# Kernel optimization log

Hardware: AMD Instinct MI355X
Metric: run time of the kernel (lower is better)

## Reference

```python
import jax, jax.numpy as jnp
import numpy as np

N, IN_DIM, H, D = 4096, 512, 8, 64
NEG = -1e9  # additive mask value for non-edges


def setup_inputs() -> dict:
    key = jax.random.key(0)
    k1, k2, k3, k4, k5, k6 = jax.random.split(key, 6)
    data = jax.random.normal(k1, (N, IN_DIM), dtype=jnp.float32)
    r = jax.random.uniform(k2, (N, N), dtype=jnp.float32)
    connectivity = jnp.where(r < 0.05, 0.0, NEG).astype(jnp.float32)
    # xavier-uniform-ish init for params
    lim_w = float(np.sqrt(6.0 / (IN_DIM + H * D)))
    W = jax.random.uniform(k3, (H * D, IN_DIM), jnp.float32, -lim_w, lim_w)
    b = jnp.zeros((H * D,), jnp.float32)
    lim_p = float(np.sqrt(6.0 / (H * D + 1)))
    src_proj = jax.random.uniform(k4, (1, H, D), jnp.float32, -lim_p, lim_p)
    trg_proj = jax.random.uniform(k5, (1, H, D), jnp.float32, -lim_p, lim_p)
    return {"data": data, "connectivity": connectivity, "W": W, "b": b,
            "src_proj": src_proj, "trg_proj": trg_proj}


def reference(data, connectivity, W, b, src_proj, trg_proj):
    # dropout is identity in eval mode (reference is deterministic)
    data1 = (data @ W.T + b).reshape(N, H, D)          # (N,H,D)
    src = jnp.einsum('nhd,xhd->nh', data1, src_proj)   # (N,H)
    trg = jnp.einsum('nhd,xhd->nh', data1, trg_proj)   # (N,H)
    # scores: (H,N,1) + (H,1,N) broadcast outer-sum
    e = src.T[:, :, None] + trg.T[:, None, :]          # (H,N,N)
    e = jnp.where(e >= 0, e, 0.01 * e)                 # LeakyReLU(0.01)
    e = e + connectivity[None, :, :]                   # additive mask
    scores = jax.nn.softmax(e, axis=-1)                # (H,N,N)
    # bmm over heads: (H,N,N) x (H,N,D) -> (H,N,D)
    out = jnp.einsum('hnm,hmd->hnd', scores, data1.transpose(1, 0, 2))
    out = out.transpose(1, 0, 2).reshape(N, H * D)     # concat=True
    return out
```

## Files before the change

kernel.cpp:

```cpp
#include <hip/hip_runtime.h>
#include <hip/hip_bf16.h>

#define NN 4096
#define IN_DIM 512
#define NH 8
#define DD 64
#define HD 512
#define LOG2E 1.4426950408889634f
#define CAST_WGS 2304
#define SCAN_WGS 1024


typedef __attribute__((ext_vector_type(8))) short short8;
typedef __attribute__((ext_vector_type(4))) float f32x4;

static __device__ __forceinline__ unsigned short f2bf(float x) {
    __hip_bfloat16 h = __float2bfloat16(x);
    return *reinterpret_cast<unsigned short*>(&h);
}

static __device__ __forceinline__ unsigned cvtpk_bf16(float a, float b) {
    unsigned r;
    asm("v_cvt_pk_bf16_f32 %0, %1, %2" : "=v"(r) : "v"(a), "v"(b));
    return r;
}

__global__ __launch_bounds__(256) void k_cast_scan(const float* __restrict__ inA,
                                                   unsigned short* __restrict__ outA,
                                                   int n4A,
                                                   const float* __restrict__ inB,
                                                   unsigned short* __restrict__ outB,
                                                   int n4B,
                                                   const float* __restrict__ conn,
                                                   unsigned long long* __restrict__ bm) {
    if (blockIdx.x >= CAST_WGS) {
        const int lane = threadIdx.x & 63;
        const int w = threadIdx.x >> 6;
        const int row = (blockIdx.x - CAST_WGS) * 4 + w;
        const float* crow = conn + (size_t)row * NN;
        unsigned long long keep = 0;
#pragma unroll 8
        for (int t = 0; t < 64; t++) {
            float c = crow[t * 64 + lane];
            unsigned long long m = __ballot(c == 0.0f);
            if (lane == t) keep = m;
        }
        bm[(size_t)row * 64 + lane] = keep;
        return;
    }
    int t = blockIdx.x * 256 + threadIdx.x;
    const float* in;
    unsigned short* out;
    if (t < n4A) {
        in = inA; out = outA;
    } else {
        t -= n4A;
        if (t >= n4B) return;
        in = inB; out = outB;
    }
    float4 v = ((const float4*)in)[t];
    ushort4 o;
    o.x = f2bf(v.x); o.y = f2bf(v.y); o.z = f2bf(v.z); o.w = f2bf(v.w);
    ((ushort4*)out)[t] = o;
}

__global__ __launch_bounds__(512) void k_gemm_fused(const unsigned short* __restrict__ Ab,
                                                    const unsigned short* __restrict__ Wb,
                                                    const float* __restrict__ bias,
                                                    const float* __restrict__ sp,
                                                    const float* __restrict__ tp,
                                                    unsigned short* __restrict__ d1t,
                                                    float* __restrict__ srcT,
                                                    float* __restrict__ trgT) {
    __shared__ f32x4 cbuf[4][4 * 64];
    const int lane = threadIdx.x & 63;
    const int w8 = threadIdx.x >> 6;
    const int w  = w8 & 3;
    const int kh = w8 >> 2;
    const int col = lane & 15;
    const int quad = lane >> 4;
    const int koff = quad * 8 + kh * 256;
    const int h = blockIdx.x;
    const int m0 = h * 64;
    const int n0 = blockIdx.y * 64;

    const short8* ap  = (const short8*)(Ab + (size_t)(n0 + w * 16 + col) * IN_DIM + koff);
    const short8* bp0 = (const short8*)(Wb + (size_t)(m0 +  0 + col) * IN_DIM + koff);
    const short8* bp1 = (const short8*)(Wb + (size_t)(m0 + 16 + col) * IN_DIM + koff);
    const short8* bp2 = (const short8*)(Wb + (size_t)(m0 + 32 + col) * IN_DIM + koff);
    const short8* bp3 = (const short8*)(Wb + (size_t)(m0 + 48 + col) * IN_DIM + koff);

    f32x4 acc0 = {0.f, 0.f, 0.f, 0.f}, acc1 = acc0, acc2 = acc0, acc3 = acc0;

#pragma unroll 8
    for (int ks = 0; ks < 8; ks++) {
        short8 a  = ap[ks * 4];
        short8 b0 = bp0[ks * 4];
        short8 b1 = bp1[ks * 4];
        short8 b2 = bp2[ks * 4];
        short8 b3 = bp3[ks * 4];
        acc0 = __builtin_amdgcn_mfma_f32_16x16x32_bf16(a, b0, acc0, 0, 0, 0);
        acc1 = __builtin_amdgcn_mfma_f32_16x16x32_bf16(a, b1, acc1, 0, 0, 0);
        acc2 = __builtin_amdgcn_mfma_f32_16x16x32_bf16(a, b2, acc2, 0, 0, 0);
        acc3 = __builtin_amdgcn_mfma_f32_16x16x32_bf16(a, b3, acc3, 0, 0, 0);
    }

    if (kh == 1) {
        cbuf[w][0 * 64 + lane] = acc0;
        cbuf[w][1 * 64 + lane] = acc1;
        cbuf[w][2 * 64 + lane] = acc2;
        cbuf[w][3 * 64 + lane] = acc3;
    }
    __syncthreads();
    if (kh == 1) return;
    acc0 += cbuf[w][0 * 64 + lane];
    acc1 += cbuf[w][1 * 64 + lane];
    acc2 += cbuf[w][2 * 64 + lane];
    acc3 += cbuf[w][3 * 64 + lane];

    const int rbase = n0 + w * 16 + quad * 4;
    const int jt  = (n0 >> 5) + (w >> 1);
    const int kqf = ((w & 1) << 1) + (quad >> 1);
    const int half = quad & 1;
    f32x4 accs[4] = {acc0, acc1, acc2, acc3};
    float ps[4] = {0.f, 0.f, 0.f, 0.f};
    float pt[4] = {0.f, 0.f, 0.f, 0.f};
#pragma unroll
    for (int mt = 0; mt < 4; mt++) {
        const int m = m0 + mt * 16 + col;
        const float bv  = bias[m];
        const float spv = sp[m];
        const float tpv = tp[m];
        ushort4 pack;
        unsigned short* pk = (unsigned short*)&pack;
#pragma unroll
        for (int r = 0; r < 4; r++) {
            float v = accs[mt][r] + bv;
            pk[r] = f2bf(v);
            ps[r] += v * spv;
            pt[r] += v * tpv;
        }
        size_t boff = ((((size_t)(h * 128 + jt) * 4 + mt) * 64 + kqf * 16 + col) << 4)
                    + ((size_t)half << 3);
        *(ushort4*)((char*)d1t + boff) = pack;
    }
#pragma unroll
    for (int off = 1; off <= 8; off <<= 1) {
#pragma unroll
        for (int r = 0; r < 4; r++) {
            ps[r] += __shfl_xor(ps[r], off, 64);
            pt[r] += __shfl_xor(pt[r], off, 64);
        }
    }
    if (col < 4)
        srcT[(size_t)h * NN + rbase + col] = ps[col] * LOG2E;
    else if (col < 8)
        trgT[(size_t)h * NN + rbase + col - 4] = pt[col - 4] * LOG2E;
}

__global__ __launch_bounds__(512) void k_flash(const unsigned* __restrict__ bm32,
                                               const float* __restrict__ srcT,
                                               const float* __restrict__ trgT,
                                               const unsigned short* __restrict__ d1t,
                                               float* __restrict__ out) {
    __shared__ char vt[2][16384];

    const int t = threadIdx.x;
    const int lane = t & 63;
    const int w = t >> 6;
    const int col = lane & 15;
    const int kq = lane >> 4;
    const int i0 = blockIdx.x * 128;
    const int h = blockIdx.y;
    const int m = i0 + w * 16 + col;

    const float s = srcT[(size_t)h * NN + m];
    const unsigned* bp = bm32 + (size_t)m * 128;
    const float* tpp = trgT + (size_t)h * NN + kq * 8;
    const uint4* gv = (const uint4*)d1t + (size_t)h * 32768;
    const short8 ONES = {0x3F80, 0x3F80, 0x3F80, 0x3F80, 0x3F80, 0x3F80, 0x3F80, 0x3F80};

    f32x4 acc0 = {0.f, 0.f, 0.f, 0.f}, acc1 = acc0, acc2 = acc0, acc3 = acc0;
    f32x4 asum = acc0;

    {
        uint4 a0 = gv[t];
        uint4 a1 = gv[t + 512];
        *(uint4*)(vt[0] + (size_t)t * 16) = a0;
        *(uint4*)(vt[0] + (size_t)(t + 512) * 16) = a1;
    }
    uint4 st0 = gv[1024 + t];
    uint4 st1 = gv[1024 + t + 512];
    uint4 bq_c = *(const uint4*)(bp);
    uint4 bq_n = *(const uint4*)(bp + 4);
    float4 tAc[4], tBc[4], tAn[4], tBn[4];
#pragma unroll
    for (int jtl = 0; jtl < 4; jtl++) {
        tAc[jtl] = *(const float4*)(tpp + jtl * 32);
        tBc[jtl] = *(const float4*)(tpp + jtl * 32 + 4);
        tAn[jtl] = *(const float4*)(tpp + (4 + jtl) * 32);
        tBn[jtl] = *(const float4*)(tpp + (4 + jtl) * 32 + 4);
    }
    __syncthreads();

#pragma unroll 2
    for (int step = 0; step < 32; step++) {
        const int cur = step & 1;
        char* wb = vt[cur ^ 1];
        *(uint4*)(wb + (size_t)t * 16) = st0;
        *(uint4*)(wb + (size_t)(t + 512) * 16) = st1;
        const int s2 = (step + 2 < 32) ? step + 2 : 31;
        st0 = gv[s2 * 1024 + t];
        st1 = gv[s2 * 1024 + t + 512];

        const unsigned bqa[4] = {bq_c.x, bq_c.y, bq_c.z, bq_c.w};
#pragma unroll
        for (int jtl = 0; jtl < 4; jtl++) {
            const unsigned bits = (bqa[jtl] >> (kq * 8)) & 0xffu;
            const float tv[8] = {tAc[jtl].x, tAc[jtl].y, tAc[jtl].z, tAc[jtl].w,
                                 tBc[jtl].x, tBc[jtl].y, tBc[jtl].z, tBc[jtl].w};
            float p[8];
#pragma unroll
            for (int r = 0; r < 8; r++) {
                float e = s + tv[r];
                e = fmaxf(e, 0.01f * e);
                float pv = __builtin_amdgcn_exp2f(e);
                pv *= (float)((bits >> r) & 1u);
                p[r] = pv;
            }
            union { uint4 u; short8 s8; } pk;
            pk.u.x = cvtpk_bf16(p[0], p[1]);
            pk.u.y = cvtpk_bf16(p[2], p[3]);
            pk.u.z = cvtpk_bf16(p[4], p[5]);
            pk.u.w = cvtpk_bf16(p[6], p[7]);
            const char* cb = vt[cur] + jtl * 4096 + lane * 16;
            short8 v0 = *(const short8*)(cb);
            short8 v1 = *(const short8*)(cb + 1024);
            short8 v2 = *(const short8*)(cb + 2048);
            short8 v3 = *(const short8*)(cb + 3072);
            acc0 = __builtin_amdgcn_mfma_f32_16x16x32_bf16(pk.s8, v0, acc0, 0, 0, 0);
            acc1 = __builtin_amdgcn_mfma_f32_16x16x32_bf16(pk.s8, v1, acc1, 0, 0, 0);
            acc2 = __builtin_amdgcn_mfma_f32_16x16x32_bf16(pk.s8, v2, acc2, 0, 0, 0);
            acc3 = __builtin_amdgcn_mfma_f32_16x16x32_bf16(pk.s8, v3, acc3, 0, 0, 0);
            asum = __builtin_amdgcn_mfma_f32_16x16x32_bf16(pk.s8, ONES, asum, 0, 0, 0);
        }

        bq_c = bq_n;
#pragma unroll
        for (int jtl = 0; jtl < 4; jtl++) { tAc[jtl] = tAn[jtl]; tBc[jtl] = tBn[jtl]; }
        bq_n = *(const uint4*)(bp + s2 * 4);
#pragma unroll
        for (int jtl = 0; jtl < 4; jtl++) {
            tAn[jtl] = *(const float4*)(tpp + (s2 * 4 + jtl) * 32);
            tBn[jtl] = *(const float4*)(tpp + (s2 * 4 + jtl) * 32 + 4);
        }
        __syncthreads();
    }

    f32x4 accs[4] = {acc0, acc1, acc2, acc3};
#pragma unroll
    for (int r = 0; r < 4; r++) {
        const int row = i0 + w * 16 + kq * 4 + r;
        const float dv = asum[r];
        const float inv = (dv > 0.f) ? (1.f / dv) : 0.f;
        float* op = out + (size_t)row * HD + h * 64;
#pragma unroll
        for (int dt = 0; dt < 4; dt++)
            op[dt * 16 + col] = accs[dt][r] * inv;
    }
}

extern "C" void kernel_launch(void* const* d_in, const int* in_sizes, int n_in,
                              void* d_out, int out_size, void* d_ws, size_t ws_size,
                              hipStream_t stream) {
    const float* data = (const float*)d_in[0];
    const float* conn = (const float*)d_in[1];
    const float* W    = (const float*)d_in[2];
    const float* bias = (const float*)d_in[3];
    const float* sp   = (const float*)d_in[4];
    const float* tp   = (const float*)d_in[5];
    float* out = (float*)d_out;

    unsigned short* d1t = (unsigned short*)d_ws;
    unsigned short* Ab  = d1t + (size_t)HD * NN;
    unsigned short* Wb  = Ab + (size_t)NN * IN_DIM;
    float* srcT = (float*)(Wb + (size_t)HD * IN_DIM);
    float* trgT = srcT + NH * NN;
    unsigned long long* bm = (unsigned long long*)(trgT + NH * NN);

    const int n4A = NN * IN_DIM / 4;
    const int n4B = HD * IN_DIM / 4;
    k_cast_scan<<<dim3(CAST_WGS + SCAN_WGS), 256, 0, stream>>>(data, Ab, n4A, W, Wb, n4B,
                                                               conn, bm);
    k_gemm_fused<<<dim3(NH, NN / 64), 512, 0, stream>>>(Ab, Wb, bias, sp, tp,
                                                        d1t, srcT, trgT);
    k_flash<<<dim3(NN / 128, NH), 512, 0, stream>>>((const unsigned*)bm, srcT, trgT, d1t, out);
}
```

Measured before the change: 183.6 us.

## Stream V tiles directly to LDS with global_load_lds and raise MFMA priority

Replaces the register-staged global→LDS copy of the value tiles with direct global_load_lds (16-byte) into the alternate LDS buffer, prefetching one step ahead instead of two. Bitmask and target-score prefetch is restructured into ping-pong register sets via a manually unrolled macro, and the MFMA block is wrapped in s_setprio to favor matrix issue. The aim is to cut VGPR pressure and VALU/LDS-store work for staging. The trade-off is a shorter prefetch distance, with load latency now covered by one step rather than two.

New measurement: 184.9 us. No clear change (+0.7%).

```diff
diff --git a/kernel.cpp b/kernel.cpp
--- a/kernel.cpp
+++ b/kernel.cpp
@@ -14,6 +14,9 @@
 typedef __attribute__((ext_vector_type(8))) short short8;
 typedef __attribute__((ext_vector_type(4))) float f32x4;
 
+typedef __attribute__((address_space(1))) const unsigned int gu32;
+typedef __attribute__((address_space(3))) unsigned int lu32;
+
 static __device__ __forceinline__ unsigned short f2bf(float x) {
     __hip_bfloat16 h = __float2bfloat16(x);
     return *reinterpret_cast<unsigned short*>(&h);
@@ -23,6 +26,10 @@
     unsigned r;
     asm("v_cvt_pk_bf16_f32 %0, %1, %2" : "=v"(r) : "v"(a), "v"(b));
     return r;
+}
+
+static __device__ __forceinline__ void gload_lds16(const void* g, void* l) {
+    __builtin_amdgcn_global_load_lds((gu32*)g, (lu32*)l, 16, 0, 0);
 }
 
 __global__ __launch_bounds__(256) void k_cast_scan(const float* __restrict__ inA,
@@ -158,6 +165,55 @@
         trgT[(size_t)h * NN + rbase + col - 4] = pt[col - 4] * LOG2E;
 }
 
+#define FLASH_STEP(STEPN, RBASE, WDST, BQU, TAU, TBU, BQL, TAL, TBL)               \
+    do {                                                                           \
+        const int s1_ = ((STEPN) + 1 < 32) ? (STEPN) + 1 : 31;                     \
+        const uint4* gsrc_ = gw + (size_t)s1_ * 1024;                              \
+        gload_lds16(gsrc_, (WDST));                                                \
+        gload_lds16(gsrc_ + 512, (WDST) + 8192);                                   \
+        BQL = *(const uint4*)(bp + s1_ * 4);                                       \
+        _Pragma("unroll")                                                          \
+        for (int j_ = 0; j_ < 4; j_++) {                                           \
+            TAL[j_] = *(const float4*)(tpp + (s1_ * 4 + j_) * 32);                 \
+            TBL[j_] = *(const float4*)(tpp + (s1_ * 4 + j_) * 32 + 4);             \
+        }                                                                          \
+        const unsigned bqa_[4] = {BQU.x, BQU.y, BQU.z, BQU.w};                     \
+        _Pragma("unroll")                                                          \
+        for (int jtl_ = 0; jtl_ < 4; jtl_++) {                                     \
+            const unsigned bits_ = (bqa_[jtl_] >> (kq * 8)) & 0xffu;               \
+            const float tv_[8] = {TAU[jtl_].x, TAU[jtl_].y, TAU[jtl_].z,           \
+                                  TAU[jtl_].w, TBU[jtl_].x, TBU[jtl_].y,           \
+                                  TBU[jtl_].z, TBU[jtl_].w};                       \
+            float p_[8];                                                           \
+            _Pragma("unroll")                                                      \
+            for (int r_ = 0; r_ < 8; r_++) {                                       \
+                float e_ = s + tv_[r_];                                            \
+                e_ = fmaxf(e_, 0.01f * e_);                                        \
+                float pv_ = __builtin_amdgcn_exp2f(e_);                            \
+                pv_ *= (float)((bits_ >> r_) & 1u);                                \
+                p_[r_] = pv_;                                                      \
+            }                                                                      \
+            union { uint4 u; short8 s8; } pk_;                                     \
+            pk_.u.x = cvtpk_bf16(p_[0], p_[1]);                                    \
+            pk_.u.y = cvtpk_bf16(p_[2], p_[3]);                                    \
+            pk_.u.z = cvtpk_bf16(p_[4], p_[5]);                                    \
+            pk_.u.w = cvtpk_bf16(p_[6], p_[7]);                                    \
+            const char* cb_ = (RBASE) + jtl_ * 4096 + lane * 16;                   \
+            short8 v0_ = *(const short8*)(cb_);                                    \
+            short8 v1_ = *(const short8*)(cb_ + 1024);                             \
+            short8 v2_ = *(const short8*)(cb_ + 2048);                             \
+            short8 v3_ = *(const short8*)(cb_ + 3072);                             \
+            __builtin_amdgcn_s_setprio(1);                                         \
+            acc0 = __builtin_amdgcn_mfma_f32_16x16x32_bf16(pk_.s8, v0_, acc0, 0, 0, 0); \
+            acc1 = __builtin_amdgcn_mfma_f32_16x16x32_bf16(pk_.s8, v1_, acc1, 0, 0, 0); \
+            acc2 = __builtin_amdgcn_mfma_f32_16x16x32_bf16(pk_.s8, v2_, acc2, 0, 0, 0); \
+            acc3 = __builtin_amdgcn_mfma_f32_16x16x32_bf16(pk_.s8, v3_, acc3, 0, 0, 0); \
+            asum = __builtin_amdgcn_mfma_f32_16x16x32_bf16(pk_.s8, ONES, asum, 0, 0, 0); \
+            __builtin_amdgcn_s_setprio(0);                                         \
+        }                                                                          \
+        __syncthreads();                                                           \
+    } while (0)
+
 __global__ __launch_bounds__(512) void k_flash(const unsigned* __restrict__ bm32,
                                                const float* __restrict__ srcT,
                                                const float* __restrict__ trgT,
@@ -178,83 +234,30 @@
     const unsigned* bp = bm32 + (size_t)m * 128;
     const float* tpp = trgT + (size_t)h * NN + kq * 8;
     const uint4* gv = (const uint4*)d1t + (size_t)h * 32768;
+    const uint4* gw = gv + w * 64 + lane;
+    char* l0 = vt[0] + w * 1024;
+    char* l1 = vt[1] + w * 1024;
     const short8 ONES = {0x3F80, 0x3F80, 0x3F80, 0x3F80, 0x3F80, 0x3F80, 0x3F80, 0x3F80};
 
     f32x4 acc0 = {0.f, 0.f, 0.f, 0.f}, acc1 = acc0, acc2 = acc0, acc3 = acc0;
     f32x4 asum = acc0;
 
-    {
-        uint4 a0 = gv[t];
-        uint4 a1 = gv[t + 512];
-        *(uint4*)(vt[0] + (size_t)t * 16) = a0;
-        *(uint4*)(vt[0] + (size_t)(t + 512) * 16) = a1;
-    }
-    uint4 st0 = gv[1024 + t];
-    uint4 st1 = gv[1024 + t + 512];
-    uint4 bq_c = *(const uint4*)(bp);
-    uint4 bq_n = *(const uint4*)(bp + 4);
-    float4 tAc[4], tBc[4], tAn[4], tBn[4];
-#pragma unroll
-    for (int jtl = 0; jtl < 4; jtl++) {
-        tAc[jtl] = *(const float4*)(tpp + jtl * 32);
-        tBc[jtl] = *(const float4*)(tpp + jtl * 32 + 4);
-        tAn[jtl] = *(const float4*)(tpp + (4 + jtl) * 32);
-        tBn[jtl] = *(const float4*)(tpp + (4 + jtl) * 32 + 4);
+    uint4 bqA, bqB;
+    float4 tAA[4], tBA[4], tAB[4], tBB[4];
+
+    gload_lds16(gw, l0);
+    gload_lds16(gw + 512, l0 + 8192);
+    bqA = *(const uint4*)(bp);
+#pragma unroll
+    for (int j = 0; j < 4; j++) {
+        tAA[j] = *(const float4*)(tpp + j * 32);
+        tBA[j] = *(const float4*)(tpp + j * 32 + 4);
     }
     __syncthreads();
 
-#pragma unroll 2
-    for (int step = 0; step < 32; step++) {
-        const int cur = step & 1;
-        char* wb = vt[cur ^ 1];
-        *(uint4*)(wb + (size_t)t * 16) = st0;
-        *(uint4*)(wb + (size_t)(t + 512) * 16) = st1;
-        const int s2 = (step + 2 < 32) ? step + 2 : 31;
-        st0 = gv[s2 * 1024 + t];
-        st1 = gv[s2 * 1024 + t + 512];
-
-        const unsigned bqa[4] = {bq_c.x, bq_c.y, bq_c.z, bq_c.w};
-#pragma unroll
-        for (int jtl = 0; jtl < 4; jtl++) {
-            const unsigned bits = (bqa[jtl] >> (kq * 8)) & 0xffu;
-            const float tv[8] = {tAc[jtl].x, tAc[jtl].y, tAc[jtl].z, tAc[jtl].w,
-                                 tBc[jtl].x, tBc[jtl].y, tBc[jtl].z, tBc[jtl].w};
-            float p[8];
-#pragma unroll
-            for (int r = 0; r < 8; r++) {
-                float e = s + tv[r];
-                e = fmaxf(e, 0.01f * e);
-                float pv = __builtin_amdgcn_exp2f(e);
-                pv *= (float)((bits >> r) & 1u);
-                p[r] = pv;
-            }
-            union { uint4 u; short8 s8; } pk;
-            pk.u.x = cvtpk_bf16(p[0], p[1]);
-            pk.u.y = cvtpk_bf16(p[2], p[3]);
-            pk.u.z = cvtpk_bf16(p[4], p[5]);
-            pk.u.w = cvtpk_bf16(p[6], p[7]);
-            const char* cb = vt[cur] + jtl * 4096 + lane * 16;
-            short8 v0 = *(const short8*)(cb);
-            short8 v1 = *(const short8*)(cb + 1024);
-            short8 v2 = *(const short8*)(cb + 2048);
-            short8 v3 = *(const short8*)(cb + 3072);
-            acc0 = __builtin_amdgcn_mfma_f32_16x16x32_bf16(pk.s8, v0, acc0, 0, 0, 0);
-            acc1 = __builtin_amdgcn_mfma_f32_16x16x32_bf16(pk.s8, v1, acc1, 0, 0, 0);
-            acc2 = __builtin_amdgcn_mfma_f32_16x16x32_bf16(pk.s8, v2, acc2, 0, 0, 0);
-            acc3 = __builtin_amdgcn_mfma_f32_16x16x32_bf16(pk.s8, v3, acc3, 0, 0, 0);
-            asum = __builtin_amdgcn_mfma_f32_16x16x32_bf16(pk.s8, ONES, asum, 0, 0, 0);
-        }
-
-        bq_c = bq_n;
-#pragma unroll
-        for (int jtl = 0; jtl < 4; jtl++) { tAc[jtl] = tAn[jtl]; tBc[jtl] = tBn[jtl]; }
-        bq_n = *(const uint4*)(bp + s2 * 4);
-#pragma unroll
-        for (int jtl = 0; jtl < 4; jtl++) {
-            tAn[jtl] = *(const float4*)(tpp + (s2 * 4 + jtl) * 32);
-            tBn[jtl] = *(const float4*)(tpp + (s2 * 4 + jtl) * 32 + 4);
-        }
-        __syncthreads();
+    for (int it = 0; it < 16; it++) {
+        FLASH_STEP(2 * it,     vt[0], l1, bqA, tAA, tBA, bqB, tAB, tBB);
+        FLASH_STEP(2 * it + 1, vt[1], l0, bqB, tAB, tBB, bqA, tAA, tBA);
     }
 
     f32x4 accs[4] = {acc0, acc1, acc2, acc3};
```
